# Optimization experiments

Hardware: AMD Instinct MI355X
Metric: run time of the kernel (lower is better)

The kernel has to match this reference:

```python
import jax, jax.numpy as jnp
import numpy as np

B, K, E = 8192, 16, 64          # subgraphs, nodes/subgraph, edges/subgraph
FIN, FOUT = 300, 64
ALPHA, BETA = 1.0, 0.6
EPS = 1e-12


def _l2n(x):
    # F.normalize(x, p=2, dim=-1)
    return x / jnp.maximum(jnp.linalg.norm(x, axis=-1, keepdims=True), EPS)


def _flat(idx):
    # local node ids -> global ids in the batched graph (offset b*K)
    return (idx + (jnp.arange(B, dtype=idx.dtype) * K)[:, None]).ravel()


def _spmm(src_f, dst_f, w, x):
    # h[dst] += w * x[src]  over all B*E edges; x: [B,K,F]
    F = x.shape[-1]
    xf = x.reshape(B * K, F)
    msg = xf[src_f] * w.ravel()[:, None]
    return jnp.zeros((B * K, F), x.dtype).at[dst_f].add(msg).reshape(B, K, F)


def _deg_inv_sqrt(idx_f):
    d = jnp.zeros((B * K,), jnp.float32).at[idx_f].add(1.0)
    return jnp.clip(d, 1.0) ** -0.5


def _enc(feat, src, dst, w, W, b):
    # OneLayerGCNWithGlobalAdg: zero anchor feat, GraphConv(norm='none', edge_weight), ReLU
    anchor_out = jax.nn.relu(feat[:, 0, :] @ W + b)          # [B,FOUT]
    fz = feat.at[:, 0, :].set(0.0)
    x = fz @ W                                               # [B,K,FOUT]
    h = jax.nn.relu(_spmm(_flat(src), _flat(dst), w, x) + b)
    pool = h.mean(axis=1)                                    # mean over all K nodes
    return _l2n(h), _l2n(pool), _l2n(anchor_out)


def _dec(h, src, dst, w, W, b):
    # OneLayerGCN: GraphConv(norm='both', edge_weight), ReLU
    sf, df = _flat(src), _flat(dst)
    nsrc = _deg_inv_sqrt(sf).reshape(B, K, 1)   # out-degree^-1/2
    ndst = _deg_inv_sqrt(df).reshape(B, K, 1)   # in-degree^-1/2
    x = (h * nsrc) @ W                          # project first (FOUT < FIN)
    hd = jax.nn.relu(_spmm(sf, df, w, x) * ndst + b)
    pool = hd[:, :-1, :].mean(axis=1)           # mean over nodes [:-1]
    anchor = hd[:, 0, :]
    return _l2n(hd), _l2n(pool), _l2n(anchor)


def setup_inputs() -> dict:
    key = jax.random.key(0)
    ks = jax.random.split(key, 16)
    g_enc = float(np.sqrt(6.0 / (FIN + FOUT)))
    g_dec = float(np.sqrt(6.0 / (FOUT + FIN)))
    g_bil = float(np.sqrt(6.0 / (FOUT + FOUT)))
    inp = {
        'feat_p1': jax.random.normal(ks[0], (B, K, FIN), jnp.float32),
        'feat_p2': jax.random.normal(ks[1], (B, K, FIN), jnp.float32),
        'feat_n':  jax.random.normal(ks[2], (B, K, FIN), jnp.float32),
        'w_p1': jax.random.uniform(ks[3], (B, E), jnp.float32),
        'w_p2': jax.random.uniform(ks[4], (B, E), jnp.float32),
        'w_n':  jax.random.uniform(ks[5], (B, E), jnp.float32),
        'W_enc': jax.random.uniform(ks[6], (FIN, FOUT), jnp.float32, -g_enc, g_enc),
        'b_enc': jnp.zeros((FOUT,), jnp.float32),
        'W_dec': jax.random.uniform(ks[7], (FOUT, FIN), jnp.float32, -g_dec, g_dec),
        'b_dec': jnp.zeros((FIN,), jnp.float32),
        'W_bil': jax.random.uniform(ks[8], (FOUT, FOUT), jnp.float32, -g_bil, g_bil),
        'b_bil': jnp.zeros((1,), jnp.float32),
        'src_p1': jax.random.randint(ks[9], (B, E), 0, K, jnp.int32),
        'dst_p1': jax.random.randint(ks[10], (B, E), 0, K, jnp.int32),
        'src_p2': jax.random.randint(ks[11], (B, E), 0, K, jnp.int32),
        'dst_p2': jax.random.randint(ks[12], (B, E), 0, K, jnp.int32),
        'src_n':  jax.random.randint(ks[13], (B, E), 0, K, jnp.int32),
        'dst_n':  jax.random.randint(ks[14], (B, E), 0, K, jnp.int32),
    }
    return inp


def reference(feat_p1, feat_p2, feat_n, w_p1, w_p2, w_n,
              W_enc, b_enc, W_dec, b_dec, W_bil, b_bil,
              src_p1, dst_p1, src_p2, dst_p2, src_n, dst_n):
    ori1 = feat_p1[:, 0, :]
    ori2 = feat_p2[:, 0, :]

    h1, pool1, a1 = _enc(feat_p1, src_p1, dst_p1, w_p1, W_enc, b_enc)
    h2, pool2, a2 = _enc(feat_p2, src_p2, dst_p2, w_p2, W_enc, b_enc)
    _, pooln, _ = _enc(feat_n, src_n, dst_n, w_n, W_enc, b_enc)

    def disc(r, a):  # nn.Bilinear(FOUT, FOUT, 1)
        return jnp.einsum('bj,jk,bk->b', r, W_bil, a)[:, None] + b_bil

    ps1 = jax.nn.sigmoid(disc(pool1, a1))
    ps2 = jax.nn.sigmoid(disc(pool2, a2))
    ns1 = jax.nn.sigmoid(disc(pooln, a1))
    ns2 = jax.nn.sigmoid(disc(pooln, a2))

    _, _, da1 = _dec(h1, src_p1, dst_p1, w_p1, W_dec, b_dec)
    _, _, da2 = _dec(h2, src_p2, dst_p2, w_p2, W_dec, b_dec)

    m1 = jnp.mean(jnp.log(ps1) + jnp.log(1.0 - ns1))
    m2 = jnp.mean(jnp.log(ps2) + jnp.log(1.0 - ns2))
    L_con = -((m1 / 2 + m2 / 2) / 2)
    L_gen = (jnp.mean(jnp.square(da1 - ori1)) + jnp.mean(jnp.square(da2 - ori2))) / 2
    L = ALPHA * L_con + BETA * L_gen

    attributes_num = jnp.sqrt(jnp.float32(FIN))
    contr = (ns1 - ps1 + 1.0) / 2 + (ns2 - ps2 + 1.0) / 2          # [B,1]
    gen = (jnp.linalg.norm(da1 - ori1) / attributes_num / 2
           + jnp.linalg.norm(da2 - ori2) / attributes_num / 2)      # scalar
    single_predict_scores = ALPHA * contr + BETA * gen
    return L, single_predict_scores
```

## Files before the change

kernel.cpp:

```cpp
#include <hip/hip_runtime.h>

#define BB 8192
#define KK 16
#define EE 64
#define FINN 300

typedef __attribute__((ext_vector_type(8))) short short8;
typedef __attribute__((ext_vector_type(4))) float f32x4;

__device__ __forceinline__ unsigned short bf16r(float x) {
  return __builtin_bit_cast(unsigned short, (__bf16)x);
}
__device__ __forceinline__ unsigned packbf(float a, float b) {
  return (unsigned)bf16r(a) | ((unsigned)bf16r(b) << 16);
}
__device__ __forceinline__ float redC(float v) {
  v += __shfl_xor(v, 1); v += __shfl_xor(v, 2);
  v += __shfl_xor(v, 4); v += __shfl_xor(v, 8);
  return v;
}
__device__ __forceinline__ float redQ(float v) {
  v += __shfl_xor(v, 16); v += __shfl_xor(v, 32);
  return v;
}
__device__ __forceinline__ float waveSum(float v) {
#pragma unroll
  for (int off = 32; off; off >>= 1) v += __shfl_xor(v, off);
  return v;
}
__device__ __forceinline__ double waveSumD(double v) {
#pragma unroll
  for (int off = 32; off; off >>= 1) v += __shfl_xor(v, off);
  return v;
}
__device__ __forceinline__ float logsig(float z) {
  return fminf(z, 0.f) - log1pf(expf(-fabsf(z)));
}

__global__ void prep_kernel(const float* __restrict__ Wenc, uint4* __restrict__ wB) {
  const int id = blockIdx.x * 256 + threadIdx.x;
  if (id >= 2560) return;
  const int lane = id & 63;
  const int step = (id >> 6) % 10;
  const int nt = id / 640;
  const int n = nt * 16 + (lane & 15);
  const int kb = step * 32 + (lane >> 4) * 8;
  float f[8];
#pragma unroll
  for (int j2 = 0; j2 < 8; ++j2) {
    const int k = kb + j2;
    f[j2] = (k < FINN) ? Wenc[k * 64 + n] : 0.f;
  }
  uint4 o;
  o.x = packbf(f[0], f[1]); o.y = packbf(f[2], f[3]);
  o.z = packbf(f[4], f[5]); o.w = packbf(f[6], f[7]);
  wB[id] = o;
}

__global__ __launch_bounds__(256, 6) void enc_kernel(
    const float* __restrict__ fpn, const float* __restrict__ fp1, const float* __restrict__ fp2,
    const float* __restrict__ wn, const float* __restrict__ w1, const float* __restrict__ w2,
    const int* __restrict__ sn, const int* __restrict__ s1, const int* __restrict__ s2,
    const int* __restrict__ dn, const int* __restrict__ d1, const int* __restrict__ d2,
    const uint4* __restrict__ wB, const float* __restrict__ benc,
    float* __restrict__ pooln, float* __restrict__ pool1, float* __restrict__ pool2,
    float* __restrict__ a1o, float* __restrict__ a2o,
    float* __restrict__ g1o, float* __restrict__ g2o,
    float* __restrict__ nd1o, float* __restrict__ nd2o)
{
  __shared__ char smem[25856];
  unsigned* featU = (unsigned*)smem;
  char* xBc = smem;
  float* AdjL = (float*)(smem + 16384);
  char* AdjBc = smem + 20480;
  float* coefL = (float*)(smem + 24576);
  float* xAnch = (float*)(smem + 24832);

  const int tid = threadIdx.x, lane = tid & 63, wv = tid >> 6;
  const int q = lane >> 4, c = lane & 15;
  const int kf = blockIdx.x >> 11;
  const int bg = blockIdx.x & 2047;
  const int b0 = bg * 4;

  const float* feat; const float* wedg; const int* src; const int* dst;
  float* pool_out; float* a_out; float* g_out; float* nd0_out;
  if (kf == 0) {
    feat = fpn; wedg = wn; src = sn; dst = dn;
    pool_out = pooln; a_out = nullptr; g_out = nullptr; nd0_out = nullptr;
  } else if (kf == 1) {
    feat = fp1; wedg = w1; src = s1; dst = d1;
    pool_out = pool1; a_out = a1o; g_out = g1o; nd0_out = nd1o;
  } else {
    feat = fp2; wedg = w2; src = s2; dst = d2;
    pool_out = pool2; a_out = a2o; g_out = g2o; nd0_out = nd2o;
  }

  uint4 bfr[10];
  {
    const uint4* p = wB + (wv * 10) * 64 + lane;
#pragma unroll
    for (int s = 0; s < 10; ++s) bfr[s] = p[s * 64];
  }
  const float4* gf = (const float4*)(feat + (size_t)b0 * (KK * FINN));

  for (int it = tid; it < 2400; it += 256) {
    const float4 v = gf[it];
    const int row = it / 75, c4 = it - row * 75;
    uint2 o;
    o.x = packbf(v.x, v.y);
    o.y = packbf(v.z, v.w);
    *(uint2*)&featU[row * 160 + ((c4 * 2) ^ ((row & 7) << 2))] = o;
  }
  for (int it = tid; it < 320; it += 256) {
    const int row = it / 10, dlog = 150 + (it - row * 10);
    featU[row * 160 + (dlog ^ ((row & 7) << 2))] = 0;
  }
  __syncthreads();

  f32x4 acc[4];
#pragma unroll
  for (int m = 0; m < 4; ++m) acc[m] = (f32x4){0.f, 0.f, 0.f, 0.f};
  const int xr = (c & 7) << 4;

#pragma unroll
  for (int s = 0; s < 10; ++s) {
    const short8 b8 = *(const short8*)&bfr[s];
#pragma unroll
    for (int m = 0; m < 2; ++m) {
      const short8 a8 = *(const short8*)(smem + (m * 16 + c) * 640 + ((s * 64 + q * 16) ^ xr));
      acc[m] = __builtin_amdgcn_mfma_f32_16x16x32_bf16(a8, b8, acc[m], 0, 0, 0);
    }
  }
  __syncthreads();

  for (int it = tid; it < 2400; it += 256) {
    const float4 v = gf[2400 + it];
    const int row = it / 75, c4 = it - row * 75;
    uint2 o;
    o.x = packbf(v.x, v.y);
    o.y = packbf(v.z, v.w);
    *(uint2*)&featU[row * 160 + ((c4 * 2) ^ ((row & 7) << 2))] = o;
  }
  __syncthreads();

#pragma unroll
  for (int s = 0; s < 10; ++s) {
    const short8 b8 = *(const short8*)&bfr[s];
#pragma unroll
    for (int m = 2; m < 4; ++m) {
      const short8 a8 = *(const short8*)(smem + ((m - 2) * 16 + c) * 640 + ((s * 64 + q * 16) ^ xr));
      acc[m] = __builtin_amdgcn_mfma_f32_16x16x32_bf16(a8, b8, acc[m], 0, 0, 0);
    }
  }
  __syncthreads();

#pragma unroll
  for (int m = 0; m < 4; ++m) {
    unsigned* dp = (unsigned*)(xBc + ((m * 4 + wv) * 64 + (q >> 1) * 16 + c) * 16 + (q & 1) * 8);
    dp[0] = packbf(acc[m][0], acc[m][1]);
    dp[1] = packbf(acc[m][2], acc[m][3]);
    if (q == 0) xAnch[m * 64 + wv * 16 + c] = acc[m][0];
  }
  {
    const uint4 z = {0, 0, 0, 0};
    for (int i = tid; i < 512; i += 256)
      ((uint4*)xBc)[(i >> 5) * 64 + 32 + (i & 31)] = z;
    for (int i = tid; i < 512; i += 256)
      ((uint4*)(smem + 16384))[i] = z;
  }
  __syncthreads();

  const int g = wv;
  const int bu = b0 + wv;
  const int se = src[bu * EE + lane];
  const int de = dst[bu * EE + lane];
  const float we = wedg[bu * EE + lane];

  float dinv_reg = 0.f;
#pragma unroll
  for (int k = 0; k < KK; ++k) {
    const int cnt = __popcll(__ballot(se == k));
    if (lane == k) dinv_reg = rsqrtf(fmaxf((float)cnt, 1.f));
  }
  if (nd0_out) {
    const int cd0 = __popcll(__ballot(de == 0));
    if (lane == 0) nd0_out[bu] = rsqrtf(fmaxf((float)cd0, 1.f));
  }
  atomicAdd(&AdjL[g * 256 + de * 16 + se], we);
  __threadfence_block();
  {
    const f32x4 v = *(const f32x4*)(AdjL + g * 256 + lane * 4);
    const float v0 = ((lane & 3) == 0) ? 0.f : v[0];
    unsigned* w = (unsigned*)(AdjBc + g * 1024 + (lane >> 2) * 64 + (lane & 3) * 8);
    w[0] = packbf(v0, v[1]);
    w[1] = packbf(v[2], v[3]);
  }
  if (g_out && lane < KK)
    coefL[g * 16 + lane] = AdjL[g * 256 + lane] * dinv_reg;
  __threadfence_block();

  const short8 aAdj = *(const short8*)(AdjBc + g * 1024 + c * 64 + q * 16);
  float bj[4], h[4][4];
#pragma unroll
  for (int nt = 0; nt < 4; ++nt) bj[nt] = benc[nt * 16 + c];
#pragma unroll
  for (int nt = 0; nt < 4; ++nt) {
    const short8 xb = *(const short8*)(xBc + ((g * 4 + nt) * 64 + lane) * 16);
    f32x4 cc = (f32x4){0.f, 0.f, 0.f, 0.f};
    cc = __builtin_amdgcn_mfma_f32_16x16x32_bf16(aAdj, xb, cc, 0, 0, 0);
#pragma unroll
    for (int r = 0; r < 4; ++r) h[nt][r] = fmaxf(cc[r] + bj[nt], 0.f);
  }

  float pl[4];
#pragma unroll
  for (int nt = 0; nt < 4; ++nt)
    pl[nt] = redQ(h[nt][0] + h[nt][1] + h[nt][2] + h[nt][3]);
  float pn2 = redC(pl[0] * pl[0] + pl[1] * pl[1] + pl[2] * pl[2] + pl[3] * pl[3]);
  const float pinv = 1.f / fmaxf(sqrtf(pn2), 1e-12f);
  if (q == 0)
#pragma unroll
    for (int nt = 0; nt < 4; ++nt)
      pool_out[(size_t)bu * 64 + nt * 16 + c] = pl[nt] * pinv;

  if (g_out) {
    float rnv[4];
#pragma unroll
    for (int r = 0; r < 4; ++r) {
      float s2 = redC(h[0][r] * h[0][r] + h[1][r] * h[1][r] +
                      h[2][r] * h[2][r] + h[3][r] * h[3][r]);
      rnv[r] = 1.f / fmaxf(sqrtf(s2), 1e-12f);
    }
    float gp[4] = {0.f, 0.f, 0.f, 0.f};
#pragma unroll
    for (int r = 0; r < 4; ++r) {
      const float cf = coefL[g * 16 + q * 4 + r] * rnv[r];
#pragma unroll
      for (int nt = 0; nt < 4; ++nt) gp[nt] = fmaf(cf, h[nt][r], gp[nt]);
    }
#pragma unroll
    for (int nt = 0; nt < 4; ++nt) gp[nt] = redQ(gp[nt]);
    if (q == 1)
#pragma unroll
      for (int nt = 0; nt < 4; ++nt)
        g_out[(size_t)bu * 64 + nt * 16 + c] = gp[nt];
  }
  if (a_out) {
    float av[4], an2 = 0.f;
#pragma unroll
    for (int nt = 0; nt < 4; ++nt) {
      av[nt] = fmaxf(xAnch[g * 64 + nt * 16 + c] + bj[nt], 0.f);
      an2 += av[nt] * av[nt];
    }
    an2 = redC(an2);
    const float ainv = 1.f / fmaxf(sqrtf(an2), 1e-12f);
    if (q == 2)
#pragma unroll
      for (int nt = 0; nt < 4; ++nt)
        a_out[(size_t)bu * 64 + nt * 16 + c] = av[nt] * ainv;
  }
}

__global__ __launch_bounds__(256) void dec_kernel(
    const float* __restrict__ g1b, const float* __restrict__ g2b,
    const float* __restrict__ nd1b, const float* __restrict__ nd2b,
    const float* __restrict__ Wdec, const float* __restrict__ bdec,
    const float* __restrict__ feat1, const float* __restrict__ feat2,
    float* __restrict__ dArr1, float* __restrict__ dArr2)
{
  __shared__ float red[4][8];
  __shared__ float invs[8];
  const int t = threadIdx.x, lane = t & 63, wv = t >> 6;
  const int b0 = blockIdx.x * 4;
  float gva[4], gvb[4], nda[4], ndb[4];
#pragma unroll
  for (int gg = 0; gg < 4; ++gg) {
    gva[gg] = g1b[(size_t)(b0 + gg) * 64 + lane];
    gvb[gg] = g2b[(size_t)(b0 + gg) * 64 + lane];
    nda[gg] = nd1b[b0 + gg];
    ndb[gg] = nd2b[b0 + gg];
  }
  const int f0 = t, f1 = t + 256;
  const bool has1 = (f1 < FINN);
  float yA0[4] = {0.f, 0.f, 0.f, 0.f}, yA1[4] = {0.f, 0.f, 0.f, 0.f};
  float yB0[4] = {0.f, 0.f, 0.f, 0.f}, yB1[4] = {0.f, 0.f, 0.f, 0.f};
  for (int jj = 0; jj < 64; ++jj) {
    const float w0 = Wdec[jj * FINN + f0];
    const float w1 = has1 ? Wdec[jj * FINN + f1] : 0.f;
#pragma unroll
    for (int gg = 0; gg < 4; ++gg) {
      const float ga = __shfl(gva[gg], jj);
      const float gb = __shfl(gvb[gg], jj);
      yA0[gg] = fmaf(ga, w0, yA0[gg]);
      yA1[gg] = fmaf(ga, w1, yA1[gg]);
      yB0[gg] = fmaf(gb, w0, yB0[gg]);
      yB1[gg] = fmaf(gb, w1, yB1[gg]);
    }
  }
  const float bd0 = bdec[f0];
  const float bd1 = has1 ? bdec[f1] : 0.f;
  float aa0[4], aa1[4], ab0[4], ab1[4];
#pragma unroll
  for (int gg = 0; gg < 4; ++gg) {
    aa0[gg] = fmaxf(yA0[gg] * nda[gg] + bd0, 0.f);
    aa1[gg] = has1 ? fmaxf(yA1[gg] * nda[gg] + bd1, 0.f) : 0.f;
    ab0[gg] = fmaxf(yB0[gg] * ndb[gg] + bd0, 0.f);
    ab1[gg] = has1 ? fmaxf(yB1[gg] * ndb[gg] + bd1, 0.f) : 0.f;
    const float sA = waveSum(aa0[gg] * aa0[gg] + aa1[gg] * aa1[gg]);
    const float sB = waveSum(ab0[gg] * ab0[gg] + ab1[gg] * ab1[gg]);
    if (lane == 0) { red[wv][gg] = sA; red[wv][4 + gg] = sB; }
  }
  __syncthreads();
  if (t < 8) invs[t] = 1.f / fmaxf(sqrtf(red[0][t] + red[1][t] + red[2][t] + red[3][t]), 1e-12f);
  __syncthreads();
  float sdA[4], sdB[4];
#pragma unroll
  for (int gg = 0; gg < 4; ++gg) {
    const float* __restrict__ ori1 = feat1 + (size_t)(b0 + gg) * KK * FINN;
    const float* __restrict__ ori2 = feat2 + (size_t)(b0 + gg) * KK * FINN;
    const float dA0 = aa0[gg] * invs[gg] - ori1[f0];
    const float dA1 = has1 ? (aa1[gg] * invs[gg] - ori1[f1]) : 0.f;
    const float dB0 = ab0[gg] * invs[4 + gg] - ori2[f0];
    const float dB1 = has1 ? (ab1[gg] * invs[4 + gg] - ori2[f1]) : 0.f;
    sdA[gg] = waveSum(dA0 * dA0 + dA1 * dA1);
    sdB[gg] = waveSum(dB0 * dB0 + dB1 * dB1);
  }
  __syncthreads();
  if (lane == 0) {
#pragma unroll
    for (int gg = 0; gg < 4; ++gg) { red[wv][gg] = sdA[gg]; red[wv][4 + gg] = sdB[gg]; }
  }
  __syncthreads();
  if (t < 4) dArr1[b0 + t] = red[0][t] + red[1][t] + red[2][t] + red[3][t];
  else if (t < 8) dArr2[b0 + t - 4] = red[0][t] + red[1][t] + red[2][t] + red[3][t];
}

__global__ __launch_bounds__(256) void bil_kernel(
    const float* __restrict__ pool1, const float* __restrict__ pool2,
    const float* __restrict__ pooln, const float* __restrict__ a1b,
    const float* __restrict__ a2b, const float* __restrict__ Wbil,
    const float* __restrict__ bbil, float* __restrict__ contr,
    float* __restrict__ tArr1, float* __restrict__ tArr2)
{
  const int tid = threadIdx.x, wv = tid >> 6, j = tid & 63;
  const int bu = blockIdx.x * 4 + wv;
  const float p1 = pool1[(size_t)bu * 64 + j];
  const float p2 = pool2[(size_t)bu * 64 + j];
  const float pn = pooln[(size_t)bu * 64 + j];
  const float A1 = a1b[(size_t)bu * 64 + j];
  const float A2 = a2b[(size_t)bu * 64 + j];
  float v1 = 0.f, v2 = 0.f, vn = 0.f;
  for (int jj = 0; jj < 64; ++jj) {
    const float wr = Wbil[jj * 64 + j];
    v1 = fmaf(__shfl(p1, jj), wr, v1);
    v2 = fmaf(__shfl(p2, jj), wr, v2);
    vn = fmaf(__shfl(pn, jj), wr, vn);
  }
  const float d11 = waveSum(v1 * A1);
  const float d22 = waveSum(v2 * A2);
  const float dn1 = waveSum(vn * A1);
  const float dn2 = waveSum(vn * A2);
  if (j == 0) {
    const float bb = bbil[0];
    const float z11 = d11 + bb, z22 = d22 + bb, zn1 = dn1 + bb, zn2 = dn2 + bb;
    const float ps1 = 1.f / (1.f + expf(-z11));
    const float ps2 = 1.f / (1.f + expf(-z22));
    const float ns1 = 1.f / (1.f + expf(-zn1));
    const float ns2 = 1.f / (1.f + expf(-zn2));
    contr[bu] = (ns1 - ps1 + 1.f) * 0.5f + (ns2 - ps2 + 1.f) * 0.5f;
    tArr1[bu] = logsig(z11) + logsig(-zn1);
    tArr2[bu] = logsig(z22) + logsig(-zn2);
  }
}

__global__ __launch_bounds__(256) void reduce_kernel(const float* __restrict__ parts,
                                                     double* __restrict__ accs)
{
  __shared__ double sred[4];
  const int t = threadIdx.x, lane = t & 63, wv = t >> 6;
  const float* __restrict__ p = parts + (size_t)blockIdx.x * BB;
  double s = 0.0;
  for (int i = t; i < BB; i += 256) s += (double)p[i];
  s = waveSumD(s);
  if (lane == 0) sred[wv] = s;
  __syncthreads();
  if (t == 0) accs[blockIdx.x] = sred[0] + sred[1] + sred[2] + sred[3];
}

__global__ void score_kernel(const double* __restrict__ accs,
                             const float* __restrict__ contr, float* __restrict__ out)
{
  const int i = blockIdx.x * blockDim.x + threadIdx.x;
  const double T1 = accs[0], T2 = accs[1], S1d = accs[2], S2d = accs[3];
  if (i == 0) {
    const double m1 = S1d / (double)BB, m2 = S2d / (double)BB;
    const double Lcon = -(m1 + m2) * 0.25;
    const double Lgen = (T1 + T2) / (2.0 * (double)BB * (double)FINN);
    out[0] = (float)(Lcon + 0.6 * Lgen);
  }
  const float genw = (float)((sqrt(T1) + sqrt(T2)) / (2.0 * sqrt((double)FINN)));
  if (i < BB) out[1 + i] = fmaf(0.6f, genw, contr[i]);
}

extern "C" void kernel_launch(void* const* d_in, const int* in_sizes, int n_in,
                              void* d_out, int out_size, void* d_ws, size_t ws_size,
                              hipStream_t stream)
{
  const float* feat_p1 = (const float*)d_in[0];
  const float* feat_p2 = (const float*)d_in[1];
  const float* feat_n  = (const float*)d_in[2];
  const float* w_p1 = (const float*)d_in[3];
  const float* w_p2 = (const float*)d_in[4];
  const float* w_n  = (const float*)d_in[5];
  const float* W_enc = (const float*)d_in[6];
  const float* b_enc = (const float*)d_in[7];
  const float* W_dec = (const float*)d_in[8];
  const float* b_dec = (const float*)d_in[9];
  const float* W_bil = (const float*)d_in[10];
  const float* b_bil = (const float*)d_in[11];
  const int* src_p1 = (const int*)d_in[12];
  const int* dst_p1 = (const int*)d_in[13];
  const int* src_p2 = (const int*)d_in[14];
  const int* dst_p2 = (const int*)d_in[15];
  const int* src_n  = (const int*)d_in[16];
  const int* dst_n  = (const int*)d_in[17];
  float* out = (float*)d_out;

  double* accs = (double*)d_ws;
  uint4* wsB = (uint4*)((char*)d_ws + 1024);
  float* fws = (float*)((char*)d_ws + 49152);
  float* pool1 = fws;
  float* pool2 = pool1 + (size_t)BB * 64;
  float* pooln = pool2 + (size_t)BB * 64;
  float* a1 = pooln + (size_t)BB * 64;
  float* a2 = a1 + (size_t)BB * 64;
  float* g1 = a2 + (size_t)BB * 64;
  float* g2 = g1 + (size_t)BB * 64;
  float* nd01 = g2 + (size_t)BB * 64;
  float* nd02 = nd01 + BB;
  float* contr = nd02 + BB;
  float* parts = contr + BB;
  float* dArr1 = parts;
  float* dArr2 = parts + BB;
  float* tArr1 = parts + 2 * BB;
  float* tArr2 = parts + 3 * BB;

  hipLaunchKernelGGL(prep_kernel, dim3(10), dim3(256), 0, stream, W_enc, wsB);
  hipLaunchKernelGGL(enc_kernel, dim3(3 * BB / 4), dim3(256), 0, stream,
                     feat_n, feat_p1, feat_p2,
                     w_n, w_p1, w_p2,
                     src_n, src_p1, src_p2,
                     dst_n, dst_p1, dst_p2,
                     wsB, b_enc,
                     pooln, pool1, pool2,
                     a1, a2, g1, g2, nd01, nd02);
  hipLaunchKernelGGL(dec_kernel, dim3(BB / 4), dim3(256), 0, stream,
                     g1, g2, nd01, nd02, W_dec, b_dec, feat_p1, feat_p2, dArr1, dArr2);
  hipLaunchKernelGGL(bil_kernel, dim3(BB / 4), dim3(256), 0, stream,
                     pool1, pool2, pooln, a1, a2, W_bil, b_bil, contr, tArr1, tArr2);
  hipLaunchKernelGGL(reduce_kernel, dim3(4), dim3(256), 0, stream, parts, accs);
  hipLaunchKernelGGL(score_kernel, dim3((BB + 255) / 256), dim3(256), 0, stream,
                     accs, contr, out);
}
```

Before: 559.0 us.

## Prefetch second feature half into registers and fuse decoder with bilinear kernel

In the encoder kernel, each thread now loads its whole row slice of features into registers. The second half of the feature tile is prefetched before the first MFMA pass so the global load overlaps with compute. Edge indices and bias loads are hoisted to the top of the kernel, and launch bounds drop from 6 to 4 waves per SIMD to make room for the larger register footprint. The decoder and bilinear discriminator kernels are merged into one launch to save a kernel launch and a pass over the pool and anchor data, at the cost of lower occupancy in the encoder.

```diff
diff --git a/kernel.cpp b/kernel.cpp
--- a/kernel.cpp
+++ b/kernel.cpp
@@ -57,7 +57,7 @@
   wB[id] = o;
 }
 
-__global__ __launch_bounds__(256, 6) void enc_kernel(
+__global__ __launch_bounds__(256, 4) void enc_kernel(
     const float* __restrict__ fpn, const float* __restrict__ fp1, const float* __restrict__ fp2,
     const float* __restrict__ wn, const float* __restrict__ w1, const float* __restrict__ w2,
     const int* __restrict__ sn, const int* __restrict__ s1, const int* __restrict__ s2,
@@ -95,25 +95,50 @@
     pool_out = pool2; a_out = a2o; g_out = g2o; nd0_out = nd2o;
   }
 
+  const int bu = b0 + wv;
+  const int se = src[bu * EE + lane];
+  const int de = dst[bu * EE + lane];
+  const float we = wedg[bu * EE + lane];
+  float bj[4];
+#pragma unroll
+  for (int nt = 0; nt < 4; ++nt) bj[nt] = benc[nt * 16 + c];
+
   uint4 bfr[10];
   {
     const uint4* p = wB + (wv * 10) * 64 + lane;
 #pragma unroll
     for (int s = 0; s < 10; ++s) bfr[s] = p[s * 64];
   }
+
   const float4* gf = (const float4*)(feat + (size_t)b0 * (KK * FINN));
-
-  for (int it = tid; it < 2400; it += 256) {
-    const float4 v = gf[it];
-    const int row = it / 75, c4 = it - row * 75;
-    uint2 o;
-    o.x = packbf(v.x, v.y);
-    o.y = packbf(v.z, v.w);
-    *(uint2*)&featU[row * 160 + ((c4 * 2) ^ ((row & 7) << 2))] = o;
-  }
-  for (int it = tid; it < 320; it += 256) {
-    const int row = it / 10, dlog = 150 + (it - row * 10);
-    featU[row * 160 + (dlog ^ ((row & 7) << 2))] = 0;
+  const int srow = tid >> 3;
+  const int sc = tid & 7;
+  const unsigned swz = (unsigned)((srow & 7) << 2);
+  unsigned* frow = featU + srow * 160;
+
+  float4 v[10];
+#pragma unroll
+  for (int u = 0; u < 10; ++u) {
+    const int c4 = sc + u * 8;
+    if (c4 < 75) v[u] = gf[srow * 75 + c4];
+  }
+#pragma unroll
+  for (int u = 0; u < 10; ++u) {
+    const int c4 = sc + u * 8;
+    if (c4 < 75) {
+      uint2 o;
+      o.x = packbf(v[u].x, v[u].y);
+      o.y = packbf(v[u].z, v[u].w);
+      *(uint2*)&frow[(unsigned)(c4 * 2) ^ swz] = o;
+    }
+  }
+  frow[(unsigned)(150 + sc) ^ swz] = 0;
+  if (sc < 2) frow[(unsigned)(158 + sc) ^ swz] = 0;
+
+#pragma unroll
+  for (int u = 0; u < 10; ++u) {
+    const int c4 = sc + u * 8;
+    if (c4 < 75) v[u] = gf[2400 + srow * 75 + c4];
   }
   __syncthreads();
 
@@ -133,13 +158,15 @@
   }
   __syncthreads();
 
-  for (int it = tid; it < 2400; it += 256) {
-    const float4 v = gf[2400 + it];
-    const int row = it / 75, c4 = it - row * 75;
-    uint2 o;
-    o.x = packbf(v.x, v.y);
-    o.y = packbf(v.z, v.w);
-    *(uint2*)&featU[row * 160 + ((c4 * 2) ^ ((row & 7) << 2))] = o;
+#pragma unroll
+  for (int u = 0; u < 10; ++u) {
+    const int c4 = sc + u * 8;
+    if (c4 < 75) {
+      uint2 o;
+      o.x = packbf(v[u].x, v[u].y);
+      o.y = packbf(v[u].z, v[u].w);
+      *(uint2*)&frow[(unsigned)(c4 * 2) ^ swz] = o;
+    }
   }
   __syncthreads();
 
@@ -171,10 +198,6 @@
   __syncthreads();
 
   const int g = wv;
-  const int bu = b0 + wv;
-  const int se = src[bu * EE + lane];
-  const int de = dst[bu * EE + lane];
-  const float we = wedg[bu * EE + lane];
 
   float dinv_reg = 0.f;
 #pragma unroll
@@ -189,20 +212,18 @@
   atomicAdd(&AdjL[g * 256 + de * 16 + se], we);
   __threadfence_block();
   {
-    const f32x4 v = *(const f32x4*)(AdjL + g * 256 + lane * 4);
-    const float v0 = ((lane & 3) == 0) ? 0.f : v[0];
+    const f32x4 v2 = *(const f32x4*)(AdjL + g * 256 + lane * 4);
+    const float v0 = ((lane & 3) == 0) ? 0.f : v2[0];
     unsigned* w = (unsigned*)(AdjBc + g * 1024 + (lane >> 2) * 64 + (lane & 3) * 8);
-    w[0] = packbf(v0, v[1]);
-    w[1] = packbf(v[2], v[3]);
+    w[0] = packbf(v0, v2[1]);
+    w[1] = packbf(v2[2], v2[3]);
   }
   if (g_out && lane < KK)
     coefL[g * 16 + lane] = AdjL[g * 256 + lane] * dinv_reg;
   __threadfence_block();
 
   const short8 aAdj = *(const short8*)(AdjBc + g * 1024 + c * 64 + q * 16);
-  float bj[4], h[4][4];
-#pragma unroll
-  for (int nt = 0; nt < 4; ++nt) bj[nt] = benc[nt * 16 + c];
+  float h[4][4];
 #pragma unroll
   for (int nt = 0; nt < 4; ++nt) {
     const short8 xb = *(const short8*)(xBc + ((g * 4 + nt) * 64 + lane) * 16);
@@ -261,17 +282,23 @@
   }
 }
 
-__global__ __launch_bounds__(256) void dec_kernel(
+__global__ __launch_bounds__(256) void decbil_kernel(
     const float* __restrict__ g1b, const float* __restrict__ g2b,
     const float* __restrict__ nd1b, const float* __restrict__ nd2b,
     const float* __restrict__ Wdec, const float* __restrict__ bdec,
     const float* __restrict__ feat1, const float* __restrict__ feat2,
-    float* __restrict__ dArr1, float* __restrict__ dArr2)
+    const float* __restrict__ pool1, const float* __restrict__ pool2,
+    const float* __restrict__ pooln, const float* __restrict__ a1b,
+    const float* __restrict__ a2b, const float* __restrict__ Wbil,
+    const float* __restrict__ bbil,
+    float* __restrict__ dArr1, float* __restrict__ dArr2,
+    float* __restrict__ contr, float* __restrict__ tArr1, float* __restrict__ tArr2)
 {
   __shared__ float red[4][8];
   __shared__ float invs[8];
   const int t = threadIdx.x, lane = t & 63, wv = t >> 6;
   const int b0 = blockIdx.x * 4;
+
   float gva[4], gvb[4], nda[4], ndb[4];
 #pragma unroll
   for (int gg = 0; gg < 4; ++gg) {
@@ -333,17 +360,8 @@
   __syncthreads();
   if (t < 4) dArr1[b0 + t] = red[0][t] + red[1][t] + red[2][t] + red[3][t];
   else if (t < 8) dArr2[b0 + t - 4] = red[0][t] + red[1][t] + red[2][t] + red[3][t];
-}
-
-__global__ __launch_bounds__(256) void bil_kernel(
-    const float* __restrict__ pool1, const float* __restrict__ pool2,
-    const float* __restrict__ pooln, const float* __restrict__ a1b,
-    const float* __restrict__ a2b, const float* __restrict__ Wbil,
-    const float* __restrict__ bbil, float* __restrict__ contr,
-    float* __restrict__ tArr1, float* __restrict__ tArr2)
-{
-  const int tid = threadIdx.x, wv = tid >> 6, j = tid & 63;
-  const int bu = blockIdx.x * 4 + wv;
+
+  const int bu = b0 + wv, j = lane;
   const float p1 = pool1[(size_t)bu * 64 + j];
   const float p2 = pool2[(size_t)bu * 64 + j];
   const float pn = pooln[(size_t)bu * 64 + j];
@@ -454,10 +472,10 @@
                      wsB, b_enc,
                      pooln, pool1, pool2,
                      a1, a2, g1, g2, nd01, nd02);
-  hipLaunchKernelGGL(dec_kernel, dim3(BB / 4), dim3(256), 0, stream,
-                     g1, g2, nd01, nd02, W_dec, b_dec, feat_p1, feat_p2, dArr1, dArr2);
-  hipLaunchKernelGGL(bil_kernel, dim3(BB / 4), dim3(256), 0, stream,
-                     pool1, pool2, pooln, a1, a2, W_bil, b_bil, contr, tArr1, tArr2);
+  hipLaunchKernelGGL(decbil_kernel, dim3(BB / 4), dim3(256), 0, stream,
+                     g1, g2, nd01, nd02, W_dec, b_dec, feat_p1, feat_p2,
+                     pool1, pool2, pooln, a1, a2, W_bil, b_bil,
+                     dArr1, dArr2, contr, tArr1, tArr2);
   hipLaunchKernelGGL(reduce_kernel, dim3(4), dim3(256), 0, stream, parts, accs);
   hipLaunchKernelGGL(score_kernel, dim3((BB + 255) / 256), dim3(256), 0, stream,
                      accs, contr, out);
```

After: 551.8 us. No clear change (-1.3%).
